# Optimization experiments

Measured on AMD Instinct MI355X. Metric: run time of the kernel, lower is better.

Reference implementation:

```python
import jax, jax.numpy as jnp
import numpy as np

B, S, E, H = 2, 2048, 2048, 16
D = E // H  # head_dim = 128


def rotate_half(x):
    x1, x2 = jnp.split(x, 2, axis=-1)
    return jnp.concatenate([-x2, x1], axis=-1)


def rope_sincos(seq_len, dim):
    inv_freq = 1.0 / (10000.0 ** (jnp.arange(0, dim, 2, dtype=jnp.float32) / dim))
    t = jnp.arange(seq_len, dtype=jnp.float32)
    freqs = jnp.outer(t, inv_freq)            # [S, D/2]
    emb = jnp.concatenate([freqs, freqs], -1)  # [S, D]
    return jnp.sin(emb), jnp.cos(emb)


def apply_rope(x, sin, cos):
    # x: [B, S, H, D]; sin/cos: [S, D] -> [1, S, 1, D]
    sin = sin[None, :, None, :]
    cos = cos[None, :, None, :]
    return x * cos + rotate_half(x) * sin


def setup_inputs() -> dict:
    key = jax.random.key(0)
    k1, k2 = jax.random.split(key)
    x = jax.random.normal(k1, (B, S, E), dtype=jnp.float32)
    # causal boolean mask [B, 1, S, S]
    mask = jnp.broadcast_to(jnp.tril(jnp.ones((S, S), dtype=bool))[None, None], (B, 1, S, S))
    # fused QKV projection weight (hk.Linear, no bias): [E, 3E]
    W_qkv = jax.random.normal(k2, (E, 3 * E), dtype=jnp.float32) / np.sqrt(E)
    return {"x": x, "mask": mask, "W_qkv": W_qkv}


def reference(x, mask, W_qkv):
    seq_len = x.shape[1]
    qkv = x @ W_qkv                               # [B, S, 3E]
    q, k, v = jnp.split(qkv, 3, axis=-1)
    q = q.reshape(-1, seq_len, H, D)
    k = k.reshape(-1, seq_len, H, D)
    v = v.reshape(-1, seq_len, H, D)
    sin, cos = rope_sincos(seq_len, D)
    q = apply_rope(q, sin, cos)
    k = apply_rope(k, sin, cos)
    attn = jnp.einsum('bqhd,bkhd->bhqk', q, k) / jnp.sqrt(jnp.float32(D))
    m = jnp.broadcast_to(mask, (mask.shape[0], H, seq_len, k.shape[1]))
    attn = jnp.where(m, attn, -jnp.inf)
    attn = jax.nn.softmax(attn, axis=-1)
    out = jnp.einsum('bhqk,bkhd->bqhd', attn, v)
    return out.reshape(-1, seq_len, H * D)
```

## Files before the change

### kernel.cpp

```cpp
#include <hip/hip_runtime.h>

typedef __bf16 bf16;
typedef __bf16 bf16x8 __attribute__((ext_vector_type(8)));
typedef __bf16 bf16x4 __attribute__((ext_vector_type(4)));
typedef float f32x4 __attribute__((ext_vector_type(4)));

#define MFMA16(a, b, c) __builtin_amdgcn_mfma_f32_16x16x32_bf16(a, b, c, 0, 0, 0)

#define Bq 2
#define Sq 2048
#define Eq 2048
#define Hq 16
#define Dq 128
#define N3E 6144

#define GLOAD_LDS16(gp, lp) \
  __builtin_amdgcn_global_load_lds( \
      (const __attribute__((address_space(1))) void*)(gp), \
      (__attribute__((address_space(3))) void*)(lp), 16, 0, 0)

__device__ __forceinline__ bf16 f2bf(float f) {
  unsigned u = __builtin_bit_cast(unsigned, f);
  u += 0x7FFFu + ((u >> 16) & 1u);
  unsigned short h = (unsigned short)(u >> 16);
  return __builtin_bit_cast(bf16, h);
}
__device__ __forceinline__ float bf2f(bf16 b) {
  unsigned short h = __builtin_bit_cast(unsigned short, b);
  return __builtin_bit_cast(float, (unsigned)h << 16);
}

__global__ __launch_bounds__(256) void convert_x(const float* __restrict__ x,
                                                 bf16* __restrict__ xb) {
  const size_t i = ((size_t)blockIdx.x * 256 + threadIdx.x) * 8;
  float4 a = *(const float4*)(x + i);
  float4 b = *(const float4*)(x + i + 4);
  bf16x8 o;
  o[0] = f2bf(a.x); o[1] = f2bf(a.y); o[2] = f2bf(a.z); o[3] = f2bf(a.w);
  o[4] = f2bf(b.x); o[5] = f2bf(b.y); o[6] = f2bf(b.z); o[7] = f2bf(b.w);
  *(bf16x8*)(xb + i) = o;
}

__global__ __launch_bounds__(256) void convert_wt(const float* __restrict__ w,
                                                  bf16* __restrict__ wt) {
  __shared__ __align__(16) bf16 T[64][72];
  const int tid = threadIdx.x;
  const int kb = blockIdx.x & 31;
  const int nb = blockIdx.x >> 5;
  const int k0 = kb * 64, n0 = nb * 64;
  {
    const int kr = tid >> 4, nc = (tid & 15) * 4;
#pragma unroll
    for (int p = 0; p < 4; ++p) {
      const int k = kr + p * 16;
      float4 v = *(const float4*)(w + (size_t)(k0 + k) * N3E + n0 + nc);
      T[nc + 0][k] = f2bf(v.x);
      T[nc + 1][k] = f2bf(v.y);
      T[nc + 2][k] = f2bf(v.z);
      T[nc + 3][k] = f2bf(v.w);
    }
  }
  __syncthreads();
#pragma unroll
  for (int q = 0; q < 2; ++q) {
    const int id = q * 256 + tid;
    const int n = id >> 3, ch = id & 7;
    bf16x8 v = *(const bf16x8*)&T[n][ch * 8];
    *(bf16x8*)(wt + (size_t)(n0 + n) * Eq + k0 + ch * 8) = v;
  }
}

__global__ __launch_bounds__(256) void gemm_qkv(
    const bf16* __restrict__ xb, const bf16* __restrict__ wt,
    bf16* __restrict__ qws, bf16* __restrict__ kws, bf16* __restrict__ vtws) {
  __shared__ __align__(16) bf16 Sm[128 * 136];
  bf16* Ald = Sm;
  bf16* Bld = Sm + 8192;

  const int tid = threadIdx.x;
  const int lane = tid & 63, wave = tid >> 6;
  const int q4 = lane >> 4, c = lane & 15;
  const int m0 = blockIdx.y * 128, n0 = blockIdx.x * 128;
  const int wm = (wave >> 1) * 64, wn = (wave & 1) * 64;

  f32x4 acc[4][4];
#pragma unroll
  for (int i = 0; i < 4; ++i)
#pragma unroll
    for (int j = 0; j < 4; ++j) acc[i][j] = {0.f, 0.f, 0.f, 0.f};

  for (int k0 = 0; k0 < Eq; k0 += 64) {
#pragma unroll
    for (int it = 0; it < 4; ++it) {
      const int slot = it * 256 + tid;
      const int chunk = slot >> 7, row = slot & 127;
      const bf16* gp = xb + (size_t)(m0 + row) * Eq + k0 + chunk * 8;
      GLOAD_LDS16(gp, Ald + slot * 8);
    }
#pragma unroll
    for (int it = 0; it < 4; ++it) {
      const int slot = it * 256 + tid;
      const int chunk = slot >> 7, row = slot & 127;
      const bf16* gp = wt + (size_t)(n0 + row) * Eq + k0 + chunk * 8;
      GLOAD_LDS16(gp, Bld + slot * 8);
    }
    __syncthreads();
#pragma unroll
    for (int kk = 0; kk < 64; kk += 32) {
      const int chunk = (kk >> 3) + q4;
      bf16x8 af[4], bfr[4];
#pragma unroll
      for (int i = 0; i < 4; ++i)
        af[i] = *(const bf16x8*)&Ald[(chunk * 128 + wm + i * 16 + c) * 8];
#pragma unroll
      for (int j = 0; j < 4; ++j)
        bfr[j] = *(const bf16x8*)&Bld[(chunk * 128 + wn + j * 16 + c) * 8];
#pragma unroll
      for (int i = 0; i < 4; ++i)
#pragma unroll
        for (int j = 0; j < 4; ++j)
          acc[i][j] = MFMA16(af[i], bfr[j], acc[i][j]);
    }
    __syncthreads();
  }

  const int t = n0 >> 11;
  const int b = m0 >> 11;
  const int s0 = m0 & 2047;
  const int h = (n0 & 2047) >> 7;

  if (t == 2) {
#pragma unroll
    for (int i = 0; i < 4; ++i)
#pragma unroll
      for (int j = 0; j < 4; ++j) {
        bf16x4 pv;
        pv[0] = f2bf(acc[i][j][0]); pv[1] = f2bf(acc[i][j][1]);
        pv[2] = f2bf(acc[i][j][2]); pv[3] = f2bf(acc[i][j][3]);
        *(bf16x4*)&Sm[(wn + j * 16 + c) * 136 + wm + i * 16 + q4 * 4] = pv;
      }
    __syncthreads();
    bf16* vbase = vtws + ((size_t)(b * Hq + h) * Dq) * Sq + s0;
#pragma unroll
    for (int p = 0; p < 8; ++p) {
      const int d = p * 16 + (tid >> 4), chunk = tid & 15;
      bf16x8 v = *(const bf16x8*)&Sm[d * 136 + chunk * 8];
      *(bf16x8*)&vbase[(size_t)d * Sq + chunk * 8] = v;
    }
  } else {
#pragma unroll
    for (int i = 0; i < 4; ++i)
#pragma unroll
      for (int j = 0; j < 4; ++j)
#pragma unroll
        for (int rr = 0; rr < 4; ++rr)
          Sm[(wm + i * 16 + q4 * 4 + rr) * 136 + wn + j * 16 + c] =
              f2bf(acc[i][j][rr]);
    __syncthreads();
    bf16* dst = ((t == 0) ? qws : kws) + ((size_t)(b * Hq + h) * Sq + s0) * Dq;
#pragma unroll
    for (int p = 0; p < 4; ++p) {
      const int row = p * 32 + (tid >> 3);
      const int dlow = (tid & 7) * 8;
      const int s = s0 + row;
      bf16x8 lo = *(const bf16x8*)&Sm[row * 136 + dlow];
      bf16x8 hi = *(const bf16x8*)&Sm[row * 136 + 64 + dlow];
      bf16x8 olo, ohi;
#pragma unroll
      for (int e = 0; e < 8; ++e) {
        const int d = dlow + e;
        const float freq = __expf(-(float)d * 0.14391157f);
        const float ang = (float)s * freq;
        float sv, cv;
        __sincosf(ang, &sv, &cv);
        const float x1 = bf2f(lo[e]), x2 = bf2f(hi[e]);
        olo[e] = f2bf(x1 * cv - x2 * sv);
        ohi[e] = f2bf(x2 * cv + x1 * sv);
      }
      *(bf16x8*)&dst[(size_t)row * Dq + dlow] = olo;
      *(bf16x8*)&dst[(size_t)row * Dq + 64 + dlow] = ohi;
    }
  }
}

__global__ __launch_bounds__(256, 2) void attn_kernel(
    const bf16* __restrict__ qws, const bf16* __restrict__ kws,
    const bf16* __restrict__ vtws, float* __restrict__ out) {
  __shared__ __align__(16) bf16 Kld[2][8192];
  __shared__ __align__(16) bf16 Vld[2][8192];
  __shared__ __align__(16) bf16 Plds[4][16][72];

  const int tid = threadIdx.x, lane = tid & 63, wave = tid >> 6;
  const int q4 = lane >> 4, c = lane & 15;
  const int h = blockIdx.y, b = blockIdx.z;
  const int qt = b ? blockIdx.x : (15 - blockIdx.x);
  const size_t bh = (size_t)(b * Hq + h);
  const bf16* qbase = qws + bh * Sq * Dq;
  const bf16* kbase = kws + bh * Sq * Dq;
  const bf16* vbase = vtws + bh * Dq * Sq;
  const int q0 = qt * 128 + wave * 32;
  const float kSc = 0.08838834764831845f * 1.4426950408889634f;

  bf16x8 qf[2][4];
#pragma unroll
  for (int g = 0; g < 2; ++g)
#pragma unroll
    for (int ks = 0; ks < 4; ++ks)
      qf[g][ks] = *(const bf16x8*)
          &qbase[(size_t)(q0 + g * 16 + c) * Dq + ks * 32 + q4 * 8];

  f32x4 Ot[2][8];
  float m_i[2], l_i[2];
#pragma unroll
  for (int g = 0; g < 2; ++g) {
#pragma unroll
    for (int dj = 0; dj < 8; ++dj) Ot[g][dj] = {0.f, 0.f, 0.f, 0.f};
    m_i[g] = -1e30f; l_i[g] = 0.f;
  }

  const int nchunks = 2 * qt + 2;

#pragma unroll
  for (int it = 0; it < 4; ++it) {
    const int slot = it * 256 + tid;
    GLOAD_LDS16(kbase + (size_t)(slot & 63) * Dq + (slot >> 6) * 8,
                &Kld[0][slot * 8]);
    GLOAD_LDS16(vbase + (size_t)(slot & 127) * Sq + (slot >> 7) * 8,
                &Vld[0][slot * 8]);
  }
  __syncthreads();

  for (int kb = 0; kb < nchunks; ++kb) {
    const int buf = kb & 1;
    if (kb + 1 < nchunks) {
      const int nb = buf ^ 1;
      const int koff = (kb + 1) * 64;
#pragma unroll
      for (int it = 0; it < 4; ++it) {
        const int slot = it * 256 + tid;
        GLOAD_LDS16(kbase + (size_t)(koff + (slot & 63)) * Dq + (slot >> 6) * 8,
                    &Kld[nb][slot * 8]);
        GLOAD_LDS16(vbase + (size_t)(slot & 127) * Sq + koff + (slot >> 7) * 8,
                    &Vld[nb][slot * 8]);
      }
    }
    const bool masked = (kb >= 2 * qt);
#pragma unroll
    for (int g = 0; g < 2; ++g) {
      const int qg = q0 + g * 16 + c;
      f32x4 st[4];
#pragma unroll
      for (int j8 = 0; j8 < 4; ++j8) st[j8] = {0.f, 0.f, 0.f, 0.f};
#pragma unroll
      for (int ks = 0; ks < 4; ++ks) {
        const bf16x8 qv = qf[g][ks];
#pragma unroll
        for (int j8 = 0; j8 < 4; ++j8) {
          const bf16x8 kv = *(const bf16x8*)
              &Kld[buf][((ks * 4 + q4) * 64 + j8 * 16 + c) * 8];
          st[j8] = MFMA16(kv, qv, st[j8]);
        }
      }
      if (masked) {
        const int kb64 = kb * 64 + q4 * 4;
#pragma unroll
        for (int j8 = 0; j8 < 4; ++j8)
#pragma unroll
          for (int rr = 0; rr < 4; ++rr)
            if (kb64 + j8 * 16 + rr > qg) st[j8][rr] = -1e30f;
      }
      float mloc = -1e30f;
#pragma unroll
      for (int j8 = 0; j8 < 4; ++j8)
#pragma unroll
        for (int rr = 0; rr < 4; ++rr) mloc = fmaxf(mloc, st[j8][rr]);
      mloc = fmaxf(mloc, __shfl_xor(mloc, 16, 64));
      mloc = fmaxf(mloc, __shfl_xor(mloc, 32, 64));
      const float mn = fmaxf(m_i[g], mloc);
      const float alpha = exp2f((m_i[g] - mn) * kSc);
      m_i[g] = mn;
      float ssum = 0.f;
#pragma unroll
      for (int j8 = 0; j8 < 4; ++j8)
#pragma unroll
        for (int rr = 0; rr < 4; ++rr) {
          const float p = exp2f((st[j8][rr] - mn) * kSc);
          st[j8][rr] = p;
          ssum += p;
        }
      ssum += __shfl_xor(ssum, 16, 64);
      ssum += __shfl_xor(ssum, 32, 64);
      l_i[g] = l_i[g] * alpha + ssum;
#pragma unroll
      for (int dj = 0; dj < 8; ++dj) Ot[g][dj] *= alpha;
#pragma unroll
      for (int j8 = 0; j8 < 4; ++j8) {
        bf16x4 pk;
        pk[0] = f2bf(st[j8][0]); pk[1] = f2bf(st[j8][1]);
        pk[2] = f2bf(st[j8][2]); pk[3] = f2bf(st[j8][3]);
        *(bf16x4*)&Plds[wave][c][j8 * 16 + q4 * 4] = pk;
      }
#pragma unroll
      for (int ks = 0; ks < 2; ++ks) {
        const bf16x8 pv = *(const bf16x8*)&Plds[wave][c][ks * 32 + q4 * 8];
#pragma unroll
        for (int dj = 0; dj < 8; ++dj) {
          const bf16x8 vv = *(const bf16x8*)
              &Vld[buf][((ks * 4 + q4) * 128 + dj * 16 + c) * 8];
          Ot[g][dj] = MFMA16(vv, pv, Ot[g][dj]);
        }
      }
    }
    __syncthreads();
  }

#pragma unroll
  for (int g = 0; g < 2; ++g) {
    const float inv = 1.0f / l_i[g];
    float* orow = out + ((size_t)b * Sq + q0 + g * 16 + c) * Eq + h * Dq;
#pragma unroll
    for (int dj = 0; dj < 8; ++dj) {
      float4 o;
      o.x = Ot[g][dj][0] * inv; o.y = Ot[g][dj][1] * inv;
      o.z = Ot[g][dj][2] * inv; o.w = Ot[g][dj][3] * inv;
      *(float4*)&orow[dj * 16 + q4 * 4] = o;
    }
  }
}

extern "C" void kernel_launch(void* const* d_in, const int* in_sizes, int n_in,
                              void* d_out, int out_size, void* d_ws,
                              size_t ws_size, hipStream_t stream) {
  const float* x = (const float*)d_in[0];
  const float* w = (const float*)d_in[2];
  float* out = (float*)d_out;

  const size_t nX = (size_t)Bq * Sq * Eq;
  const size_t nW = (size_t)Eq * N3E;
  const size_t perT = (size_t)Bq * Hq * Sq * Dq;

  bf16* xb = (bf16*)d_ws;
  bf16* wt = xb + nX;
  bf16* qws = wt + nW;
  bf16* kws = qws + perT;
  bf16* vtws = kws + perT;

  convert_x<<<nX / (256 * 8), 256, 0, stream>>>(x, xb);
  convert_wt<<<(Eq / 64) * (N3E / 64), 256, 0, stream>>>(w, wt);

  dim3 g1(N3E / 128, (Bq * Sq) / 128);
  gemm_qkv<<<g1, 256, 0, stream>>>(xb, wt, qws, kws, vtws);

  dim3 g3(Sq / 128, Hq, Bq);
  attn_kernel<<<g3, 256, 0, stream>>>(qws, kws, vtws, out);
}
```

Measured before the change: 440.3 us.

## Triple-buffer QKV GEMM with swizzled LDS, larger tiles, and precomputed RoPE table

Rewrites the QKV GEMM to use 128x256 tiles with 512 threads, a three-stage global-to-LDS pipeline with partial vmcnt waits instead of a full sync every K step, and XOR-swizzled LDS layout to avoid bank conflicts. It adds an XCD-aware block remapping and MFMA priority hints. RoPE sin/cos is moved to a small precomputed table kernel instead of per-element transcendentals in the epilogue. This costs more LDS per block (144KB for two blocks per CU) and an extra launch plus workspace for the table.

Measured after the change: 374.1 us. -15.0%, faster.

```diff
diff --git a/kernel.cpp b/kernel.cpp
--- a/kernel.cpp
+++ b/kernel.cpp
@@ -70,18 +70,32 @@
   }
 }
 
-__global__ __launch_bounds__(256) void gemm_qkv(
+__global__ __launch_bounds__(256) void rope_table(float2* __restrict__ tbl) {
+  const int i = blockIdx.x * 256 + threadIdx.x;
+  const int s = i >> 6, d = i & 63;
+  const float freq = __expf(-(float)d * 0.14391157f);
+  const float ang = (float)s * freq;
+  float sv, cv;
+  __sincosf(ang, &sv, &cv);
+  tbl[i] = make_float2(cv, sv);
+}
+
+__global__ __launch_bounds__(512, 2) void gemm_qkv(
     const bf16* __restrict__ xb, const bf16* __restrict__ wt,
-    bf16* __restrict__ qws, bf16* __restrict__ kws, bf16* __restrict__ vtws) {
-  __shared__ __align__(16) bf16 Sm[128 * 136];
-  bf16* Ald = Sm;
-  bf16* Bld = Sm + 8192;
+    const float2* __restrict__ tbl, bf16* __restrict__ qws,
+    bf16* __restrict__ kws, bf16* __restrict__ vtws) {
+  __shared__ __align__(16) bf16 LDS[3 * 24576];
 
   const int tid = threadIdx.x;
-  const int lane = tid & 63, wave = tid >> 6;
+  const int lane = tid & 63, wv = tid >> 6;
   const int q4 = lane >> 4, c = lane & 15;
-  const int m0 = blockIdx.y * 128, n0 = blockIdx.x * 128;
-  const int wm = (wave >> 1) * 64, wn = (wave & 1) * 64;
+  const int wm = (wv >> 2) * 64;
+  const int wn = (wv & 3) * 64;
+
+  const int bid = blockIdx.x;
+  const int wg = (bid & 7) * 96 + (bid >> 3);
+  const int m0 = (wg / 24) * 128;
+  const int n0 = (wg % 24) * 256;
 
   f32x4 acc[4][4];
 #pragma unroll
@@ -89,96 +103,141 @@
 #pragma unroll
     for (int j = 0; j < 4; ++j) acc[i][j] = {0.f, 0.f, 0.f, 0.f};
 
-  for (int k0 = 0; k0 < Eq; k0 += 64) {
+  const int NT = Eq / 64;
+
+  auto stage = [&](int t, int st) {
+    bf16* ab = LDS + st * 24576;
+    bf16* bb = ab + 8192;
+    const int k0 = t * 64;
+#pragma unroll
+    for (int it = 0; it < 2; ++it) {
+      const int slot = it * 512 + tid;
+      const int row = slot >> 3, kch = slot & 7;
+      const int kcs = kch ^ (row & 7);
+      GLOAD_LDS16(xb + (size_t)(m0 + row) * Eq + k0 + kcs * 8, ab + slot * 8);
+    }
 #pragma unroll
     for (int it = 0; it < 4; ++it) {
-      const int slot = it * 256 + tid;
-      const int chunk = slot >> 7, row = slot & 127;
-      const bf16* gp = xb + (size_t)(m0 + row) * Eq + k0 + chunk * 8;
-      GLOAD_LDS16(gp, Ald + slot * 8);
-    }
-#pragma unroll
-    for (int it = 0; it < 4; ++it) {
-      const int slot = it * 256 + tid;
-      const int chunk = slot >> 7, row = slot & 127;
-      const bf16* gp = wt + (size_t)(n0 + row) * Eq + k0 + chunk * 8;
-      GLOAD_LDS16(gp, Bld + slot * 8);
-    }
-    __syncthreads();
+      const int slot = it * 512 + tid;
+      const int row = slot >> 3, kch = slot & 7;
+      const int kcs = kch ^ (row & 7);
+      GLOAD_LDS16(wt + (size_t)(n0 + row) * Eq + k0 + kcs * 8, bb + slot * 8);
+    }
+  };
+
+  stage(0, 0);
+  stage(1, 1);
+  asm volatile("s_waitcnt vmcnt(6)" ::: "memory");
+  __builtin_amdgcn_s_barrier();
+
+  int stC = 0;
+#pragma unroll 1
+  for (int t = 0; t < NT; ++t) {
+    if (t + 2 < NT) {
+      int ss = stC + 2;
+      if (ss >= 3) ss -= 3;
+      stage(t + 2, ss);
+    }
+    const bf16* A = LDS + stC * 24576;
+    const bf16* Bb = A + 8192;
 #pragma unroll
     for (int kk = 0; kk < 64; kk += 32) {
-      const int chunk = (kk >> 3) + q4;
+      const int bch = kk >> 3;
       bf16x8 af[4], bfr[4];
 #pragma unroll
       for (int i = 0; i < 4; ++i)
-        af[i] = *(const bf16x8*)&Ald[(chunk * 128 + wm + i * 16 + c) * 8];
+        af[i] = *(const bf16x8*)
+            &A[(wm + i * 16 + c) * 64 + ((bch + q4) ^ (c & 7)) * 8];
 #pragma unroll
       for (int j = 0; j < 4; ++j)
-        bfr[j] = *(const bf16x8*)&Bld[(chunk * 128 + wn + j * 16 + c) * 8];
+        bfr[j] = *(const bf16x8*)
+            &Bb[(wn + j * 16 + c) * 64 + ((bch + q4) ^ (c & 7)) * 8];
+      __builtin_amdgcn_s_setprio(1);
 #pragma unroll
       for (int i = 0; i < 4; ++i)
 #pragma unroll
         for (int j = 0; j < 4; ++j)
           acc[i][j] = MFMA16(af[i], bfr[j], acc[i][j]);
-    }
-    __syncthreads();
-  }
-
-  const int t = n0 >> 11;
+      __builtin_amdgcn_s_setprio(0);
+    }
+    if (t + 1 < NT) {
+      if (t + 2 < NT) asm volatile("s_waitcnt vmcnt(6)" ::: "memory");
+      else            asm volatile("s_waitcnt vmcnt(0)" ::: "memory");
+      __builtin_amdgcn_s_barrier();
+    }
+    stC = stC == 2 ? 0 : stC + 1;
+  }
+  __syncthreads();
+
+  const int t3 = n0 >> 11;
   const int b = m0 >> 11;
   const int s0 = m0 & 2047;
-  const int h = (n0 & 2047) >> 7;
-
-  if (t == 2) {
-#pragma unroll
-    for (int i = 0; i < 4; ++i)
-#pragma unroll
-      for (int j = 0; j < 4; ++j) {
-        bf16x4 pv;
-        pv[0] = f2bf(acc[i][j][0]); pv[1] = f2bf(acc[i][j][1]);
-        pv[2] = f2bf(acc[i][j][2]); pv[3] = f2bf(acc[i][j][3]);
-        *(bf16x4*)&Sm[(wn + j * 16 + c) * 136 + wm + i * 16 + q4 * 4] = pv;
-      }
-    __syncthreads();
-    bf16* vbase = vtws + ((size_t)(b * Hq + h) * Dq) * Sq + s0;
-#pragma unroll
-    for (int p = 0; p < 8; ++p) {
-      const int d = p * 16 + (tid >> 4), chunk = tid & 15;
-      bf16x8 v = *(const bf16x8*)&Sm[d * 136 + chunk * 8];
-      *(bf16x8*)&vbase[(size_t)d * Sq + chunk * 8] = v;
+  const int h0 = (n0 & 2047) >> 7;
+
+  bf16* E = LDS;
+
+  if (t3 == 2) {
+#pragma unroll 1
+    for (int hh = 0; hh < 2; ++hh) {
+      if (((wv & 3) >> 1) == hh) {
+#pragma unroll
+        for (int i = 0; i < 4; ++i)
+#pragma unroll
+          for (int j = 0; j < 4; ++j) {
+            bf16x4 pv;
+            pv[0] = f2bf(acc[i][j][0]); pv[1] = f2bf(acc[i][j][1]);
+            pv[2] = f2bf(acc[i][j][2]); pv[3] = f2bf(acc[i][j][3]);
+            *(bf16x4*)&E[((wn & 127) + j * 16 + c) * 136 + wm + i * 16 +
+                         q4 * 4] = pv;
+          }
+      }
+      __syncthreads();
+      bf16* vbase = vtws + ((size_t)(b * Hq + h0 + hh) * Dq) * Sq + s0;
+#pragma unroll
+      for (int p = 0; p < 4; ++p) {
+        const int id = p * 512 + tid;
+        const int d = id >> 4, ch = id & 15;
+        bf16x8 v = *(const bf16x8*)&E[d * 136 + ch * 8];
+        *(bf16x8*)&vbase[(size_t)d * Sq + ch * 8] = v;
+      }
+      __syncthreads();
     }
   } else {
-#pragma unroll
-    for (int i = 0; i < 4; ++i)
-#pragma unroll
-      for (int j = 0; j < 4; ++j)
-#pragma unroll
-        for (int rr = 0; rr < 4; ++rr)
-          Sm[(wm + i * 16 + q4 * 4 + rr) * 136 + wn + j * 16 + c] =
-              f2bf(acc[i][j][rr]);
-    __syncthreads();
-    bf16* dst = ((t == 0) ? qws : kws) + ((size_t)(b * Hq + h) * Sq + s0) * Dq;
-#pragma unroll
-    for (int p = 0; p < 4; ++p) {
-      const int row = p * 32 + (tid >> 3);
-      const int dlow = (tid & 7) * 8;
-      const int s = s0 + row;
-      bf16x8 lo = *(const bf16x8*)&Sm[row * 136 + dlow];
-      bf16x8 hi = *(const bf16x8*)&Sm[row * 136 + 64 + dlow];
-      bf16x8 olo, ohi;
-#pragma unroll
-      for (int e = 0; e < 8; ++e) {
-        const int d = dlow + e;
-        const float freq = __expf(-(float)d * 0.14391157f);
-        const float ang = (float)s * freq;
-        float sv, cv;
-        __sincosf(ang, &sv, &cv);
-        const float x1 = bf2f(lo[e]), x2 = bf2f(hi[e]);
-        olo[e] = f2bf(x1 * cv - x2 * sv);
-        ohi[e] = f2bf(x2 * cv + x1 * sv);
-      }
-      *(bf16x8*)&dst[(size_t)row * Dq + dlow] = olo;
-      *(bf16x8*)&dst[(size_t)row * Dq + 64 + dlow] = ohi;
+#pragma unroll 1
+    for (int hh = 0; hh < 2; ++hh) {
+      if (((wv & 3) >> 1) == hh) {
+#pragma unroll
+        for (int i = 0; i < 4; ++i)
+#pragma unroll
+          for (int j = 0; j < 4; ++j)
+#pragma unroll
+            for (int rr = 0; rr < 4; ++rr)
+              E[(wm + i * 16 + q4 * 4 + rr) * 136 + (wn & 127) + j * 16 + c] =
+                  f2bf(acc[i][j][rr]);
+      }
+      __syncthreads();
+      bf16* hd = ((t3 == 0) ? qws : kws) +
+                 ((size_t)(b * Hq + h0 + hh) * Sq + s0) * Dq;
+#pragma unroll
+      for (int p = 0; p < 2; ++p) {
+        const int row = p * 64 + (tid >> 3);
+        const int dlow = (tid & 7) * 8;
+        const int s = s0 + row;
+        bf16x8 lo = *(const bf16x8*)&E[row * 136 + dlow];
+        bf16x8 hi = *(const bf16x8*)&E[row * 136 + 64 + dlow];
+        const float2* tb = tbl + (size_t)s * 64 + dlow;
+        bf16x8 olo, ohi;
+#pragma unroll
+        for (int e = 0; e < 8; ++e) {
+          const float cv = tb[e].x, sv = tb[e].y;
+          const float x1 = bf2f(lo[e]), x2 = bf2f(hi[e]);
+          olo[e] = f2bf(x1 * cv - x2 * sv);
+          ohi[e] = f2bf(x2 * cv + x1 * sv);
+        }
+        *(bf16x8*)&hd[(size_t)row * Dq + dlow] = olo;
+        *(bf16x8*)&hd[(size_t)row * Dq + 64 + dlow] = ohi;
+      }
+      __syncthreads();
     }
   }
 }
@@ -344,12 +403,13 @@
   bf16* qws = wt + nW;
   bf16* kws = qws + perT;
   bf16* vtws = kws + perT;
+  float2* tbl = (float2*)(vtws + perT);
 
   convert_x<<<nX / (256 * 8), 256, 0, stream>>>(x, xb);
   convert_wt<<<(Eq / 64) * (N3E / 64), 256, 0, stream>>>(w, wt);
-
-  dim3 g1(N3E / 128, (Bq * Sq) / 128);
-  gemm_qkv<<<g1, 256, 0, stream>>>(xb, wt, qws, kws, vtws);
+  rope_table<<<(Sq * 64) / 256, 256, 0, stream>>>(tbl);
+
+  gemm_qkv<<<768, 512, 0, stream>>>(xb, wt, tbl, qws, kws, vtws);
 
   dim3 g3(Sq / 128, Hq, Bq);
   attn_kernel<<<g3, 256, 0, stream>>>(qws, kws, vtws, out);
```
